# Performance work log

Hardware: AMD Instinct MI355X
Metric: run time of the kernel (lower is better)

The kernel has to match this reference:

```python
import jax, jax.numpy as jnp
import numpy as np

DIM = 1024
HEADS = 16
HEAD_DIM = DIM // HEADS
WINDOW = 128


def setup_inputs() -> dict:
    key = jax.random.key(0)
    k1, k2, k3, k4 = jax.random.split(key, 4)
    B, T = 2, 2048
    x = jax.random.normal(k1, (B, T, DIM), dtype=jnp.float32)
    # nn.Linear(dim, 3*dim, bias=False): weight [3*dim, dim]; y = x @ W.T
    W_qkv = jax.random.normal(k2, (3 * DIM, DIM), dtype=jnp.float32) * (1.0 / np.sqrt(DIM))
    W_proj = jax.random.normal(k3, (DIM, DIM), dtype=jnp.float32) * (1.0 / np.sqrt(DIM))
    b_proj = jax.random.normal(k4, (DIM,), dtype=jnp.float32) * 0.01
    return {"x": x, "W_qkv": W_qkv, "W_proj": W_proj, "b_proj": b_proj}


def reference(x, W_qkv, W_proj, b_proj) -> jnp.ndarray:
    B, T, C = x.shape
    scale = HEAD_DIM ** -0.5
    qkv = jnp.einsum('btc,oc->bto', x, W_qkv)  # [B,T,3*D]
    qkv = qkv.reshape(B, T, 3, HEADS, HEAD_DIM)
    qkv = jnp.transpose(qkv, (2, 0, 3, 1, 4))  # [3,B,H,T,hd]
    q, k, v = qkv[0], qkv[1], qkv[2]
    # sliding-window mask: attend iff |i-j| <= WINDOW
    idx = jnp.arange(T)
    mask = jnp.abs(idx[:, None] - idx[None, :]) <= WINDOW  # [T,T]
    scores = jnp.einsum('bhqd,bhkd->bhqk', q, k) * scale  # [B,H,T,T]
    scores = jnp.where(mask[None, None], scores, jnp.finfo(scores.dtype).min)
    attn = jax.nn.softmax(scores, axis=-1)
    out = jnp.einsum('bhqk,bhkd->bhqd', attn, v)  # [B,H,T,hd]
    out = jnp.transpose(out, (0, 2, 1, 3)).reshape(B, T, C)
    return jnp.einsum('btc,oc->bto', out, W_proj) + b_proj
```

## Files before the change

kernel.cpp:

```cpp
#include <hip/hip_runtime.h>
#include <hip/hip_bf16.h>
#include <cstdint>
#include <cstddef>

#define DIMC 1024
#define HEADS 16
#define HD 64
#define WINDOW 128
#define BB 2
#define TT 2048
#define NTOK (BB*TT)
#define QKVN (3*DIMC)

typedef __bf16 bf16;
typedef __bf16 bf16x8 __attribute__((ext_vector_type(8)));
typedef __bf16 bf16x4 __attribute__((ext_vector_type(4)));
typedef float f32x4 __attribute__((ext_vector_type(4)));
typedef unsigned int u32;

typedef const __attribute__((address_space(1))) u32* gp1_t;
typedef __attribute__((address_space(3))) u32* lp3_t;

__device__ __forceinline__ void gload16(const void* g, void* l) {
  __builtin_amdgcn_global_load_lds((gp1_t)g, (lp3_t)l, 16, 0, 0);
}

__device__ __forceinline__ void BAR() {
  asm volatile("" ::: "memory");
  __builtin_amdgcn_s_barrier();
  asm volatile("" ::: "memory");
}

__global__ void cast3_kernel(const float* __restrict__ x,
                             const float* __restrict__ wq,
                             const float* __restrict__ wp,
                             bf16* __restrict__ xo,
                             bf16* __restrict__ wqo,
                             bf16* __restrict__ wpo) {
  const int NX = NTOK * DIMC / 4;
  const int NQ = QKVN * DIMC / 4;
  const int NP = DIMC * DIMC / 4;
  const int total = NX + NQ + NP;
  typedef float float4v __attribute__((ext_vector_type(4)));
  for (int i = blockIdx.x * blockDim.x + threadIdx.x; i < total;
       i += gridDim.x * blockDim.x) {
    const float4v* src; bf16* dst; int j;
    if (i < NX)            { src = (const float4v*)x;  dst = xo;  j = i; }
    else if (i < NX + NQ)  { src = (const float4v*)wq; dst = wqo; j = i - NX; }
    else                   { src = (const float4v*)wp; dst = wpo; j = i - NX - NQ; }
    float4v v = src[j];
    bf16x4 o;
    o[0] = (bf16)v[0]; o[1] = (bf16)v[1]; o[2] = (bf16)v[2]; o[3] = (bf16)v[3];
    ((bf16x4*)dst)[j] = o;
  }
}

__device__ __forceinline__ bf16x8 lds_frag(const bf16* base, int row, int colb) {
  const char* p = (const char*)base + row * 128 + (colb ^ ((row & 7) << 4));
  return *(const bf16x8*)p;
}

__global__ __launch_bounds__(512, 2) void gemm256_qkv_kernel(
    const bf16* __restrict__ A, const bf16* __restrict__ Bw,
    bf16* __restrict__ C) {
  constexpr int K = 1024;
  constexpr int NT = K / 64;
  __shared__ bf16 Alds[2][256 * 64];
  __shared__ bf16 Blds[2][192 * 64];

  const int tid = threadIdx.x;
  const int wid = tid >> 6, l = tid & 63;
  const int wm = wid >> 2, wn = wid & 3;
  const int lr = l & 15, lg = l >> 4;
  const int w8 = wid * 8;

  const int bid = blockIdx.x;
  const int wg = (bid & 7) * 32 + (bid >> 3);
  const int bm = wg & 15;
  const int bn = wg >> 4;

  const char* Ag = (const char*)A + (size_t)(bm * 256) * 2048;
  const char* Bg = (const char*)Bw + (size_t)(bn * 192) * 2048;

  auto stageA = [&](bf16* lds, int kt, int half) {
#pragma unroll
    for (int i = 0; i < 2; i++) {
      const int R0 = half * 64 + i * 128 + w8;
      const int r = R0 + (l >> 3);
      const char* src = Ag + (size_t)r * 2048 + kt * 128
                        + (((l & 7) * 16) ^ ((r & 7) << 4));
      gload16(src, lds + R0 * 64);
    }
  };
  auto stageB = [&](bf16* lds, int kt, int third) {
    const int R0 = third * 64 + w8;
    const int r = R0 + (l >> 3);
    const char* src = Bg + (size_t)r * 2048 + kt * 128
                      + (((l & 7) * 16) ^ ((r & 7) << 4));
    gload16(src, lds + R0 * 64);
  };

  stageB(Blds[0], 0, 0); stageB(Blds[0], 0, 1); stageB(Blds[0], 0, 2);
  stageA(Alds[0], 0, 0); stageA(Alds[0], 0, 1);
  stageB(Blds[1], 1, 0); stageB(Blds[1], 1, 1); stageB(Blds[1], 1, 2);
  stageA(Alds[1], 1, 0);
  asm volatile("s_waitcnt vmcnt(5)" ::: "memory");
  BAR();

  f32x4 acc[8][3] = {};

  auto ktile = [&](int kt, const bf16* Acur, const bf16* Bcur,
                   bf16* Anext, bf16* Acur_w, bf16* Bcur_w) {
    bf16x8 bfr[3][2];
    bf16x8 afr[2][2], afn[2][2];
#pragma unroll
    for (int n = 0; n < 3; n++)
#pragma unroll
      for (int kk = 0; kk < 2; kk++)
        bfr[n][kk] = lds_frag(Bcur, wn * 48 + n * 16 + lr, kk * 64 + lg * 16);
#pragma unroll
    for (int mi = 0; mi < 2; mi++)
#pragma unroll
      for (int kk = 0; kk < 2; kk++)
        afr[mi][kk] = lds_frag(Acur, wm * 128 + mi * 16 + lr, kk * 64 + lg * 16);

#pragma unroll
    for (int mq = 0; mq < 4; ++mq) {
      if (mq < 3) {
#pragma unroll
        for (int mi = 0; mi < 2; mi++)
#pragma unroll
          for (int kk = 0; kk < 2; kk++)
            afn[mi][kk] = lds_frag(Acur, wm * 128 + (2 * (mq + 1) + mi) * 16 + lr,
                                   kk * 64 + lg * 16);
      }
      if (mq == 0)      { if (kt + 1 < NT) stageA(Anext,  kt + 1, 1); }
      else if (mq == 1) { if (kt + 2 < NT) stageB(Bcur_w, kt + 2, 0); }
      else if (mq == 2) { if (kt + 2 < NT) { stageB(Bcur_w, kt + 2, 1);
                                             stageB(Bcur_w, kt + 2, 2); } }
      else              { if (kt + 2 < NT) stageA(Acur_w, kt + 2, 0); }
      __builtin_amdgcn_s_setprio(1);
#pragma unroll
      for (int kk = 0; kk < 2; kk++)
#pragma unroll
        for (int mi = 0; mi < 2; mi++)
#pragma unroll
          for (int n = 0; n < 3; n++)
            acc[2 * mq + mi][n] = __builtin_amdgcn_mfma_f32_16x16x32_bf16(
                afr[mi][kk], bfr[n][kk], acc[2 * mq + mi][n], 0, 0, 0);
      __builtin_amdgcn_s_setprio(0);
      if (mq == 3) {
        if (kt >= NT - 2) asm volatile("s_waitcnt vmcnt(0)" ::: "memory");
        else              asm volatile("s_waitcnt vmcnt(5)" ::: "memory");
      }
      BAR();
      if (mq < 3) {
#pragma unroll
        for (int mi = 0; mi < 2; mi++)
#pragma unroll
          for (int kk = 0; kk < 2; kk++)
            afr[mi][kk] = afn[mi][kk];
      }
    }
  };

  for (int kt2 = 0; kt2 < NT; kt2 += 2) {
    ktile(kt2,     Alds[0], Blds[0], Alds[1], Alds[0], Blds[0]);
    ktile(kt2 + 1, Alds[1], Blds[1], Alds[0], Alds[1], Blds[1]);
  }

#pragma unroll
  for (int m = 0; m < 8; m++) {
    const int row = bm * 256 + wm * 128 + m * 16 + lg * 4;
#pragma unroll
    for (int n = 0; n < 3; n++) {
      const int col = bn * 192 + wn * 48 + n * 16 + lr;
#pragma unroll
      for (int j = 0; j < 4; j++)
        C[(size_t)(row + j) * QKVN + col] = (bf16)acc[m][n][j];
    }
  }
}

template<int N_>
__global__ __launch_bounds__(256, 2) void gemm_bt_kernel(
    const bf16* __restrict__ A, const bf16* __restrict__ Bw,
    float* __restrict__ Cf, const float* __restrict__ bias) {
  constexpr int K = 1024;
  constexpr int KB = K * 2;
  __shared__ bf16 As[2][128 * 32];
  __shared__ bf16 Bs[2][128 * 32];

  const int tid = threadIdx.x;
  const int w = tid >> 6, l = tid & 63;
  const int bm = blockIdx.x & 31;
  const int bn = blockIdx.x >> 5;
  const int wm = w >> 1, wn = w & 1;
  const int lr = l & 15, lg = l >> 4;

  const int srow = w * 32 + (l >> 2);
  const int scolb = (l & 3) * 16;
  const char* Agb = (const char*)A + (size_t)(bm * 128 + srow) * KB + scolb;
  const char* Bgb = (const char*)Bw + (size_t)(bn * 128 + srow) * KB + scolb;

  f32x4 acc[4][4] = {};

  auto stage = [&](int buf, int t) {
    const char* ag = Agb + t * 64;
    const char* bg = Bgb + t * 64;
    gload16(ag,            &As[buf][(w * 32) * 32]);
    gload16(ag + 16 * KB,  &As[buf][(w * 32 + 16) * 32]);
    gload16(bg,            &Bs[buf][(w * 32) * 32]);
    gload16(bg + 16 * KB,  &Bs[buf][(w * 32 + 16) * 32]);
  };

  stage(0, 0);
  __syncthreads();
  constexpr int NTiles = K / 32;
  int buf = 0;
  for (int t = 0; t < NTiles; ++t) {
    if (t + 1 < NTiles) stage(buf ^ 1, t + 1);
    bf16x8 af[4], bfr[4];
#pragma unroll
    for (int m = 0; m < 4; m++)
      af[m] = *(const bf16x8*)&As[buf][(wm * 64 + m * 16 + lr) * 32 + lg * 8];
#pragma unroll
    for (int n = 0; n < 4; n++)
      bfr[n] = *(const bf16x8*)&Bs[buf][(wn * 64 + n * 16 + lr) * 32 + lg * 8];
#pragma unroll
    for (int m = 0; m < 4; m++)
#pragma unroll
      for (int n = 0; n < 4; n++)
        acc[m][n] = __builtin_amdgcn_mfma_f32_16x16x32_bf16(af[m], bfr[n], acc[m][n], 0, 0, 0);
    __syncthreads();
    buf ^= 1;
  }

#pragma unroll
  for (int m = 0; m < 4; m++) {
    const int row = bm * 128 + wm * 64 + m * 16 + lg * 4;
#pragma unroll
    for (int n = 0; n < 4; n++) {
      const int col = bn * 128 + wn * 64 + n * 16 + lr;
#pragma unroll
      for (int j = 0; j < 4; j++)
        Cf[(size_t)(row + j) * N_ + col] = acc[m][n][j] + bias[col];
    }
  }
}

__global__ __launch_bounds__(256, 2) void attn_kernel(const bf16* __restrict__ qkv,
                                                      bf16* __restrict__ out) {
  __shared__ bf16 Kl[64][72];
  __shared__ bf16 Vt[64][72];
  __shared__ bf16 Pl[4][16][72];

  const int tid = threadIdx.x, w = tid >> 6, l = tid & 63;
  const int qb = blockIdx.x & 31, bh = blockIdx.x >> 5;
  const int b = bh >> 4, h = bh & 15;
  const int q0 = qb * 64;
  const int lr = l & 15, lg = l >> 4;
  const float SC = 0.18033688011f;

  bf16x8 qf[2];
  {
    const bf16* qp = qkv + (size_t)(b * TT + q0 + w * 16 + lr) * QKVN + h * HD + lg * 8;
    qf[0] = *(const bf16x8*)qp;
    qf[1] = *(const bf16x8*)(qp + 32);
  }

  f32x4 Oa[4] = {};
  float mrow[4], lrow[4];
#pragma unroll
  for (int j = 0; j < 4; j++) { mrow[j] = -1e30f; lrow[j] = 0.f; }

  int kb0 = qb - 2; if (kb0 < 0) kb0 = 0;
  int kb1 = qb + 2; if (kb1 > 31) kb1 = 31;

  for (int kb = kb0; kb <= kb1; ++kb) {
    const int kvbase = kb * 64;
#pragma unroll
    for (int task = 0; task < 2; task++) {
      int lin = tid + 256 * task;
      int r = lin >> 3, cb = lin & 7;
      const bf16* kp = qkv + (size_t)(b * TT + kvbase + r) * QKVN + DIMC + h * HD + cb * 8;
      *(bf16x8*)&Kl[r][cb * 8] = *(const bf16x8*)kp;
    }
#pragma unroll
    for (int task = 0; task < 2; task++) {
      int lin = tid + 256 * task;
      int r = lin & 63, c0 = (lin >> 6) * 8;
      bf16x8 vv = *(const bf16x8*)(qkv + (size_t)(b * TT + kvbase + r) * QKVN + 2 * DIMC + h * HD + c0);
#pragma unroll
      for (int e = 0; e < 8; e++) Vt[c0 + e][r] = vv[e];
    }
    __syncthreads();

    f32x4 Sa[4] = {};
#pragma unroll
    for (int kf = 0; kf < 2; kf++)
#pragma unroll
      for (int nf = 0; nf < 4; nf++) {
        bf16x8 kfr = *(const bf16x8*)&Kl[nf * 16 + lr][kf * 32 + lg * 8];
        Sa[nf] = __builtin_amdgcn_mfma_f32_16x16x32_bf16(qf[kf], kfr, Sa[nf], 0, 0, 0);
      }

    float mblk[4];
#pragma unroll
    for (int j = 0; j < 4; j++) mblk[j] = -1e30f;
    const int qrow_ = q0 + w * 16 + lg * 4;
#pragma unroll
    for (int nf = 0; nf < 4; nf++) {
      int kv = kvbase + nf * 16 + lr;
#pragma unroll
      for (int j = 0; j < 4; j++) {
        int dq = qrow_ + j - kv;
        float s = Sa[nf][j] * SC;
        if (dq > WINDOW || dq < -WINDOW) s = -1e30f;
        Sa[nf][j] = s;
        mblk[j] = fmaxf(mblk[j], s);
      }
    }
#pragma unroll
    for (int j = 0; j < 4; j++) {
#pragma unroll
      for (int sh = 1; sh < 16; sh <<= 1)
        mblk[j] = fmaxf(mblk[j], __shfl_xor(mblk[j], sh, 16));
    }
    float scl[4];
#pragma unroll
    for (int j = 0; j < 4; j++) {
      float mn = fmaxf(mrow[j], mblk[j]);
      scl[j] = exp2f(mrow[j] - mn);
      mrow[j] = mn;
    }
    float rsum[4] = {0.f, 0.f, 0.f, 0.f};
#pragma unroll
    for (int nf = 0; nf < 4; nf++)
#pragma unroll
      for (int j = 0; j < 4; j++) {
        float p = exp2f(Sa[nf][j] - mrow[j]);
        Sa[nf][j] = p;
        rsum[j] += p;
      }
#pragma unroll
    for (int j = 0; j < 4; j++) {
#pragma unroll
      for (int sh = 1; sh < 16; sh <<= 1)
        rsum[j] += __shfl_xor(rsum[j], sh, 16);
      lrow[j] = lrow[j] * scl[j] + rsum[j];
    }
#pragma unroll
    for (int nf = 0; nf < 4; nf++)
#pragma unroll
      for (int j = 0; j < 4; j++) Oa[nf][j] *= scl[j];

#pragma unroll
    for (int nf = 0; nf < 4; nf++)
#pragma unroll
      for (int j = 0; j < 4; j++)
        Pl[w][lg * 4 + j][nf * 16 + lr] = (bf16)Sa[nf][j];
#pragma unroll
    for (int kf = 0; kf < 2; kf++) {
      bf16x8 pf = *(const bf16x8*)&Pl[w][lr][kf * 32 + lg * 8];
#pragma unroll
      for (int nf = 0; nf < 4; nf++) {
        bf16x8 vfr = *(const bf16x8*)&Vt[nf * 16 + lr][kf * 32 + lg * 8];
        Oa[nf] = __builtin_amdgcn_mfma_f32_16x16x32_bf16(pf, vfr, Oa[nf], 0, 0, 0);
      }
    }
    __syncthreads();
  }

#pragma unroll
  for (int nf = 0; nf < 4; nf++) {
#pragma unroll
    for (int j = 0; j < 4; j++) {
      int qrow = q0 + w * 16 + lg * 4 + j;
      int d = nf * 16 + lr;
      out[(size_t)(b * TT + qrow) * DIMC + h * HD + d] = (bf16)(Oa[nf][j] / lrow[j]);
    }
  }
}

extern "C" void kernel_launch(void* const* d_in, const int* in_sizes, int n_in,
                              void* d_out, int out_size, void* d_ws, size_t ws_size,
                              hipStream_t stream) {
  const float* x     = (const float*)d_in[0];
  const float* Wqkv  = (const float*)d_in[1];
  const float* Wproj = (const float*)d_in[2];
  const float* bproj = (const float*)d_in[3];
  float* out = (float*)d_out;

  char* ws = (char*)d_ws;
  bf16* xb   = (bf16*)(ws);
  bf16* wqb  = (bf16*)(ws + 8388608);
  bf16* wpb  = (bf16*)(ws + 14680064);
  bf16* qkvb = (bf16*)(ws + 16777216);
  bf16* aob  = (bf16*)(ws + 41943040);

  cast3_kernel<<<2048, 256, 0, stream>>>(x, Wqkv, Wproj, xb, wqb, wpb);
  gemm256_qkv_kernel<<<256, 512, 0, stream>>>(xb, wqb, qkvb);
  attn_kernel<<<1024, 256, 0, stream>>>(qkvb, aob);
  gemm_bt_kernel<DIMC><<<dim3(32 * 8), 256, 0, stream>>>(aob, wpb, out, bproj);
}
```

Before: 93.44 us.

## Double-buffer attention K/V via async LDS loads and transpose reads, restructure QKV GEMM

The attention kernel now stages K and V with global_load_lds into double-buffered, swizzled shared memory, prefetching the next KV block while computing the current one. It computes S transposed so the P fragments stay in registers (removing the P round trip through LDS) and reads V with ds_read_b64_tr_b16 instead of a scalar transpose store. The occupancy hint is raised to 4 blocks per CU. Separately, the QKV GEMM k-tile loop drops A-fragment register prefetching and adds an extra barrier per sub-step, which reduces register pressure but may serialise LDS reads against MFMA work.

```diff
diff --git a/kernel.cpp b/kernel.cpp
--- a/kernel.cpp
+++ b/kernel.cpp
@@ -23,6 +23,10 @@
 
 __device__ __forceinline__ void gload16(const void* g, void* l) {
   __builtin_amdgcn_global_load_lds((gp1_t)g, (lp3_t)l, 16, 0, 0);
+}
+
+__device__ __forceinline__ u32 lds_u32(const void* p) {
+  return (u32)(uintptr_t)(__attribute__((address_space(3))) const void*)p;
 }
 
 __device__ __forceinline__ void BAR() {
@@ -112,33 +116,29 @@
   auto ktile = [&](int kt, const bf16* Acur, const bf16* Bcur,
                    bf16* Anext, bf16* Acur_w, bf16* Bcur_w) {
     bf16x8 bfr[3][2];
-    bf16x8 afr[2][2], afn[2][2];
-#pragma unroll
-    for (int n = 0; n < 3; n++)
-#pragma unroll
-      for (int kk = 0; kk < 2; kk++)
-        bfr[n][kk] = lds_frag(Bcur, wn * 48 + n * 16 + lr, kk * 64 + lg * 16);
-#pragma unroll
-    for (int mi = 0; mi < 2; mi++)
-#pragma unroll
-      for (int kk = 0; kk < 2; kk++)
-        afr[mi][kk] = lds_frag(Acur, wm * 128 + mi * 16 + lr, kk * 64 + lg * 16);
-
 #pragma unroll
     for (int mq = 0; mq < 4; ++mq) {
-      if (mq < 3) {
-#pragma unroll
-        for (int mi = 0; mi < 2; mi++)
+      bf16x8 afr[2][2];
+      if (mq == 0) {
+#pragma unroll
+        for (int n = 0; n < 3; n++)
 #pragma unroll
           for (int kk = 0; kk < 2; kk++)
-            afn[mi][kk] = lds_frag(Acur, wm * 128 + (2 * (mq + 1) + mi) * 16 + lr,
-                                   kk * 64 + lg * 16);
-      }
+            bfr[n][kk] = lds_frag(Bcur, wn * 48 + n * 16 + lr, kk * 64 + lg * 16);
+      }
+#pragma unroll
+      for (int mi = 0; mi < 2; mi++)
+#pragma unroll
+        for (int kk = 0; kk < 2; kk++)
+          afr[mi][kk] = lds_frag(Acur, wm * 128 + (2 * mq + mi) * 16 + lr,
+                                 kk * 64 + lg * 16);
       if (mq == 0)      { if (kt + 1 < NT) stageA(Anext,  kt + 1, 1); }
       else if (mq == 1) { if (kt + 2 < NT) stageB(Bcur_w, kt + 2, 0); }
       else if (mq == 2) { if (kt + 2 < NT) { stageB(Bcur_w, kt + 2, 1);
                                              stageB(Bcur_w, kt + 2, 2); } }
       else              { if (kt + 2 < NT) stageA(Acur_w, kt + 2, 0); }
+      BAR();
+      asm volatile("s_waitcnt lgkmcnt(0)" ::: "memory");
       __builtin_amdgcn_s_setprio(1);
 #pragma unroll
       for (int kk = 0; kk < 2; kk++)
@@ -154,13 +154,6 @@
         else              asm volatile("s_waitcnt vmcnt(5)" ::: "memory");
       }
       BAR();
-      if (mq < 3) {
-#pragma unroll
-        for (int mi = 0; mi < 2; mi++)
-#pragma unroll
-          for (int kk = 0; kk < 2; kk++)
-            afr[mi][kk] = afn[mi][kk];
-      }
     }
   };
 
@@ -249,11 +242,10 @@
   }
 }
 
-__global__ __launch_bounds__(256, 2) void attn_kernel(const bf16* __restrict__ qkv,
+__global__ __launch_bounds__(256, 4) void attn_kernel(const bf16* __restrict__ qkv,
                                                       bf16* __restrict__ out) {
-  __shared__ bf16 Kl[64][72];
-  __shared__ bf16 Vt[64][72];
-  __shared__ bf16 Pl[4][16][72];
+  __shared__ bf16 Kl[2][64 * 64];
+  __shared__ bf16 Vl[2][64 * 64];
 
   const int tid = threadIdx.x, w = tid >> 6, l = tid & 63;
   const int qb = blockIdx.x & 31, bh = blockIdx.x >> 5;
@@ -262,6 +254,38 @@
   const int lr = l & 15, lg = l >> 4;
   const float SC = 0.18033688011f;
 
+  const char* qkv_b = (const char*)qkv + (size_t)(b * TT) * (QKVN * 2);
+
+  size_t koff[2]; u32 kdst[2];
+#pragma unroll
+  for (int i = 0; i < 2; i++) {
+    const int R0 = 8 * (w + 4 * i);
+    const int r = R0 + (l >> 3);
+    const int colb = (((l & 7) * 16) ^ (((l >> 3) & 7) << 4));
+    koff[i] = (size_t)r * (QKVN * 2) + (DIMC + h * HD) * 2 + colb;
+    kdst[i] = (u32)(R0 * 64);
+  }
+  size_t voff[2]; u32 vdst[2];
+#pragma unroll
+  for (int i = 0; i < 2; i++) {
+    const int c = tid + 256 * i;
+    const int t = c >> 3, w_ = c & 7;
+    const int kv = (t & 15) * 4 + (w_ >> 1);
+    const int d  = (t >> 4) * 16 + (w_ & 1) * 8;
+    voff[i] = (size_t)kv * (QKVN * 2) + (2 * DIMC + h * HD + d) * 2;
+    vdst[i] = (u32)((w + 4 * i) * 512);
+  }
+
+  auto stage = [&](int buf, int kb) {
+    const char* rowb = qkv_b + (size_t)(kb * 64) * (QKVN * 2);
+#pragma unroll
+    for (int i = 0; i < 2; i++)
+      gload16(rowb + koff[i], &Kl[buf][kdst[i]]);
+#pragma unroll
+    for (int i = 0; i < 2; i++)
+      gload16(rowb + voff[i], &Vl[buf][vdst[i]]);
+  };
+
   bf16x8 qf[2];
   {
     const bf16* qp = qkv + (size_t)(b * TT + q0 + w * 16 + lr) * QKVN + h * HD + lg * 8;
@@ -270,115 +294,126 @@
   }
 
   f32x4 Oa[4] = {};
-  float mrow[4], lrow[4];
-#pragma unroll
-  for (int j = 0; j < 4; j++) { mrow[j] = -1e30f; lrow[j] = 0.f; }
+  float mrow = -1e30f, lrow = 0.f;
 
   int kb0 = qb - 2; if (kb0 < 0) kb0 = 0;
   int kb1 = qb + 2; if (kb1 > 31) kb1 = 31;
 
+  stage(0, kb0);
+  asm volatile("s_waitcnt vmcnt(0)" ::: "memory");
+  BAR();
+
   for (int kb = kb0; kb <= kb1; ++kb) {
-    const int kvbase = kb * 64;
-#pragma unroll
-    for (int task = 0; task < 2; task++) {
-      int lin = tid + 256 * task;
-      int r = lin >> 3, cb = lin & 7;
-      const bf16* kp = qkv + (size_t)(b * TT + kvbase + r) * QKVN + DIMC + h * HD + cb * 8;
-      *(bf16x8*)&Kl[r][cb * 8] = *(const bf16x8*)kp;
-    }
-#pragma unroll
-    for (int task = 0; task < 2; task++) {
-      int lin = tid + 256 * task;
-      int r = lin & 63, c0 = (lin >> 6) * 8;
-      bf16x8 vv = *(const bf16x8*)(qkv + (size_t)(b * TT + kvbase + r) * QKVN + 2 * DIMC + h * HD + c0);
-#pragma unroll
-      for (int e = 0; e < 8; e++) Vt[c0 + e][r] = vv[e];
-    }
-    __syncthreads();
-
+    const int c = (kb - kb0) & 1;
+    if (kb + 1 <= kb1) stage(c ^ 1, kb + 1);
+
+    const bf16* Kb = &Kl[c][0];
     f32x4 Sa[4] = {};
 #pragma unroll
     for (int kf = 0; kf < 2; kf++)
 #pragma unroll
       for (int nf = 0; nf < 4; nf++) {
-        bf16x8 kfr = *(const bf16x8*)&Kl[nf * 16 + lr][kf * 32 + lg * 8];
-        Sa[nf] = __builtin_amdgcn_mfma_f32_16x16x32_bf16(qf[kf], kfr, Sa[nf], 0, 0, 0);
-      }
-
-    float mblk[4];
-#pragma unroll
-    for (int j = 0; j < 4; j++) mblk[j] = -1e30f;
-    const int qrow_ = q0 + w * 16 + lg * 4;
-#pragma unroll
-    for (int nf = 0; nf < 4; nf++) {
-      int kv = kvbase + nf * 16 + lr;
+        const char* kp = (const char*)Kb + (nf * 16 + lr) * 128
+                         + ((kf * 64 + lg * 16) ^ ((lr & 7) << 4));
+        bf16x8 kfr = *(const bf16x8*)kp;
+        Sa[nf] = __builtin_amdgcn_mfma_f32_16x16x32_bf16(kfr, qf[kf], Sa[nf], 0, 0, 0);
+      }
+
+    bf16x4 tr0[4][2], tr1[4][2];
+    {
+      const u32 vbase = lds_u32(&Vl[c][0]) + l * 8;
+#pragma unroll
+      for (int nf = 0; nf < 4; nf++)
+#pragma unroll
+        for (int kf = 0; kf < 2; kf++) {
+          const u32 a = vbase + (u32)((nf * 16 + kf * 8) * 128);
+          asm volatile("ds_read_b64_tr_b16 %0, %1"
+                       : "=v"(tr0[nf][kf]) : "v"(a));
+          asm volatile("ds_read_b64_tr_b16 %0, %1 offset:512"
+                       : "=v"(tr1[nf][kf]) : "v"(a));
+        }
+    }
+
+    const int qrow = q0 + w * 16 + lr;
+    const int kvb = kb * 64;
+    float p[4][4];
+    float mblk = -1e30f;
+#pragma unroll
+    for (int nf = 0; nf < 4; nf++)
 #pragma unroll
       for (int j = 0; j < 4; j++) {
-        int dq = qrow_ + j - kv;
+        int kv = kvb + nf * 16 + lg * 4 + j;
+        int dq = qrow - kv;
         float s = Sa[nf][j] * SC;
         if (dq > WINDOW || dq < -WINDOW) s = -1e30f;
-        Sa[nf][j] = s;
-        mblk[j] = fmaxf(mblk[j], s);
-      }
-    }
+        p[nf][j] = s;
+        mblk = fmaxf(mblk, s);
+      }
+    mblk = fmaxf(mblk, __shfl_xor(mblk, 16));
+    mblk = fmaxf(mblk, __shfl_xor(mblk, 32));
+
+    float mn = fmaxf(mrow, mblk);
+    float scl = exp2f(mrow - mn);
+    mrow = mn;
+
+    float rsum = 0.f;
+#pragma unroll
+    for (int nf = 0; nf < 4; nf++)
+#pragma unroll
+      for (int j = 0; j < 4; j++) {
+        float e = exp2f(p[nf][j] - mn);
+        p[nf][j] = e;
+        rsum += e;
+      }
+    rsum += __shfl_xor(rsum, 16);
+    rsum += __shfl_xor(rsum, 32);
+    lrow = lrow * scl + rsum;
+
+    bf16x8 pa[2];
+#pragma unroll
+    for (int kf = 0; kf < 2; kf++)
+#pragma unroll
+      for (int e = 0; e < 4; e++) {
+        pa[kf][e]     = (bf16)p[2 * kf][e];
+        pa[kf][e + 4] = (bf16)p[2 * kf + 1][e];
+      }
+
 #pragma unroll
     for (int j = 0; j < 4; j++) {
-#pragma unroll
-      for (int sh = 1; sh < 16; sh <<= 1)
-        mblk[j] = fmaxf(mblk[j], __shfl_xor(mblk[j], sh, 16));
-    }
-    float scl[4];
+      float so = __shfl(scl, lg * 4 + j);
+#pragma unroll
+      for (int nf = 0; nf < 4; nf++) Oa[nf][j] *= so;
+    }
+
+    asm volatile("s_waitcnt lgkmcnt(0)" ::: "memory");
+    __builtin_amdgcn_sched_barrier(0);
+#pragma unroll
+    for (int nf = 0; nf < 4; nf++)
+#pragma unroll
+      for (int kf = 0; kf < 2; kf++) {
+        bf16x8 vb;
+#pragma unroll
+        for (int e = 0; e < 4; e++) {
+          vb[e]     = tr0[nf][kf][e];
+          vb[e + 4] = tr1[nf][kf][e];
+        }
+        Oa[nf] = __builtin_amdgcn_mfma_f32_16x16x32_bf16(pa[kf], vb, Oa[nf], 0, 0, 0);
+      }
+
+    asm volatile("s_waitcnt vmcnt(0)" ::: "memory");
+    BAR();
+  }
+
+  float lo[4];
+#pragma unroll
+  for (int j = 0; j < 4; j++) lo[j] = __shfl(lrow, lg * 4 + j);
+#pragma unroll
+  for (int nf = 0; nf < 4; nf++) {
 #pragma unroll
     for (int j = 0; j < 4; j++) {
-      float mn = fmaxf(mrow[j], mblk[j]);
-      scl[j] = exp2f(mrow[j] - mn);
-      mrow[j] = mn;
-    }
-    float rsum[4] = {0.f, 0.f, 0.f, 0.f};
-#pragma unroll
-    for (int nf = 0; nf < 4; nf++)
-#pragma unroll
-      for (int j = 0; j < 4; j++) {
-        float p = exp2f(Sa[nf][j] - mrow[j]);
-        Sa[nf][j] = p;
-        rsum[j] += p;
-      }
-#pragma unroll
-    for (int j = 0; j < 4; j++) {
-#pragma unroll
-      for (int sh = 1; sh < 16; sh <<= 1)
-        rsum[j] += __shfl_xor(rsum[j], sh, 16);
-      lrow[j] = lrow[j] * scl[j] + rsum[j];
-    }
-#pragma unroll
-    for (int nf = 0; nf < 4; nf++)
-#pragma unroll
-      for (int j = 0; j < 4; j++) Oa[nf][j] *= scl[j];
-
-#pragma unroll
-    for (int nf = 0; nf < 4; nf++)
-#pragma unroll
-      for (int j = 0; j < 4; j++)
-        Pl[w][lg * 4 + j][nf * 16 + lr] = (bf16)Sa[nf][j];
-#pragma unroll
-    for (int kf = 0; kf < 2; kf++) {
-      bf16x8 pf = *(const bf16x8*)&Pl[w][lr][kf * 32 + lg * 8];
-#pragma unroll
-      for (int nf = 0; nf < 4; nf++) {
-        bf16x8 vfr = *(const bf16x8*)&Vt[nf * 16 + lr][kf * 32 + lg * 8];
-        Oa[nf] = __builtin_amdgcn_mfma_f32_16x16x32_bf16(pf, vfr, Oa[nf], 0, 0, 0);
-      }
-    }
-    __syncthreads();
-  }
-
-#pragma unroll
-  for (int nf = 0; nf < 4; nf++) {
-#pragma unroll
-    for (int j = 0; j < 4; j++) {
-      int qrow = q0 + w * 16 + lg * 4 + j;
+      int q = q0 + w * 16 + lg * 4 + j;
       int d = nf * 16 + lr;
-      out[(size_t)(b * TT + qrow) * DIMC + h * HD + d] = (bf16)(Oa[nf][j] / lrow[j]);
+      out[(size_t)(b * TT + q) * DIMC + h * HD + d] = (bf16)(Oa[nf][j] / lo[j]);
     }
   }
 }
```

Measured after the change: 89.44 us. 4.3% less time.
